# Kernel tuning notes

Hardware: AMD Instinct MI355X
Metric: run time of the kernel (lower is better)

Reference implementation:

```python
import jax, jax.numpy as jnp
from jax import lax
import numpy as np

B, P, D = 32, 196, 2048   # batch, num_pixels (14x14), encoder_dim
A, E, H, V = 512, 512, 512, 10000  # attention_dim, embed_dim, decoder_dim, vocab
L = 21                    # max caption length -> T = 20 decode steps


def setup_inputs() -> dict:
    key = jax.random.key(0)
    ks = jax.random.split(key, 16)
    def n(k, shape, s=0.02):
        return jax.random.normal(k, shape, jnp.float32) * s
    def u(k, shape):
        return jax.random.uniform(k, shape, jnp.float32, -0.1, 0.1)
    caption_lengths = jnp.concatenate(
        [jnp.array([[L]], dtype=jnp.int32),
         jax.random.randint(ks[1], (B - 1, 1), 8, L + 1)], axis=0)
    return dict(
        encoder_out=jax.random.normal(ks[0], (B, P, D), jnp.float32) * 0.5,
        encoded_captions=jax.random.randint(ks[2], (B, L), 0, V),
        caption_lengths=caption_lengths,
        enc_att_w=n(ks[3], (D, A)), enc_att_b=jnp.zeros((A,), jnp.float32),
        dec_att_w=n(ks[4], (H, A)), dec_att_b=jnp.zeros((A,), jnp.float32),
        full_att_w=n(ks[5], (A,)), full_att_b=jnp.zeros((), jnp.float32),
        emb=u(ks[6], (V, E)),
        init_h_w=n(ks[7], (D, H)), init_h_b=jnp.zeros((H,), jnp.float32),
        init_c_w=n(ks[8], (D, H)), init_c_b=jnp.zeros((H,), jnp.float32),
        f_beta_w=n(ks[9], (H, D)), f_beta_b=jnp.zeros((D,), jnp.float32),
        lstm_w_ih=n(ks[10], (E + D, 4 * H)),
        lstm_w_hh=n(ks[11], (H, 4 * H)),
        lstm_b=jnp.zeros((4 * H,), jnp.float32),
        fc_w=u(ks[12], (H, V)), fc_b=jnp.zeros((V,), jnp.float32),
    )


def reference(encoder_out, encoded_captions, caption_lengths,
              enc_att_w, enc_att_b, dec_att_w, dec_att_b, full_att_w, full_att_b,
              emb, init_h_w, init_h_b, init_c_w, init_c_b,
              f_beta_w, f_beta_b, lstm_w_ih, lstm_w_hh, lstm_b, fc_w, fc_b):
    # sort batch by caption length, descending (matches torch .sort descending=True)
    lengths = caption_lengths[:, 0]
    sort_ind = jnp.argsort(-lengths)
    lengths = lengths[sort_ind]
    enc = encoder_out[sort_ind]                 # [B,P,D]
    caps = encoded_captions[sort_ind]           # [B,L]
    embs = emb[caps]                            # [B,L,E]

    mean_enc = enc.mean(axis=1)                 # [B,D]
    h0 = mean_enc @ init_h_w + init_h_b         # [B,H]
    c0 = mean_enc @ init_c_w + init_c_b

    # encoder branch of additive attention is constant across timesteps
    att1 = enc @ enc_att_w + enc_att_b          # [B,P,A]
    dec_lens = lengths - 1                      # [B]
    T = caps.shape[1] - 1

    def step(carry, xs):
        h, c = carry
        emb_t, t = xs                            # [B,E], scalar
        att2 = h @ dec_att_w + dec_att_b         # [B,A]
        e = jnp.einsum('bpa,a->bp', jax.nn.relu(att1 + att2[:, None, :]), full_att_w) + full_att_b
        alpha = jax.nn.softmax(e, axis=1)        # [B,P]
        awe = jnp.einsum('bpd,bp->bd', enc, alpha)
        gate = jax.nn.sigmoid(h @ f_beta_w + f_beta_b)
        awe = gate * awe                         # [B,D]
        x = jnp.concatenate([emb_t, awe], axis=-1)  # [B,E+D]
        g = x @ lstm_w_ih + h @ lstm_w_hh + lstm_b  # [B,4H] gates i,f,g,o
        i_g, f_g, g_g, o_g = jnp.split(g, 4, axis=-1)
        c_new = jax.nn.sigmoid(f_g) * c + jax.nn.sigmoid(i_g) * jnp.tanh(g_g)
        h_new = jax.nn.sigmoid(o_g) * jnp.tanh(c_new)
        preds = h_new @ fc_w + fc_b              # [B,V] (dropout = identity, eval mode)
        active = (t < dec_lens)[:, None]         # length-based batch slicing -> mask
        h = jnp.where(active, h_new, h)
        c = jnp.where(active, c_new, c)
        preds = jnp.where(active, preds, 0.0)
        alpha = jnp.where(active, alpha, 0.0)
        return (h, c), (preds, alpha)

    xs = (jnp.swapaxes(embs[:, :T], 0, 1), jnp.arange(T))
    (_, _), (preds, alphas) = lax.scan(step, (h0, c0), xs)
    predictions = jnp.swapaxes(preds, 0, 1)      # [B,T,V]
    alphas = jnp.swapaxes(alphas, 0, 1)          # [B,T,P]
    return predictions, caps, dec_lens, alphas, sort_ind
```

## Files before the change

kernel.cpp:

```cpp
#include <hip/hip_runtime.h>

#define B_ 32
#define P_ 196
#define D_ 2048
#define A_ 512
#define E_ 512
#define H_ 512
#define V_ 10000
#define L_ 21
#define T_ 20
#define PP 208

typedef unsigned short us;

struct KParams {
  const float* encoder_out; const int* captions; const int* cap_lens;
  const float* enc_att_w; const float* enc_att_b;
  const float* dec_att_w; const float* dec_att_b;
  const float* full_att_w; const float* full_att_b;
  const float* emb;
  const float* init_h_w; const float* init_h_b;
  const float* init_c_w; const float* init_c_b;
  const float* f_beta_w; const float* f_beta_b;
  const float* lstm_w_ih; const float* lstm_w_hh; const float* lstm_b;
  const float* fc_w; const float* fc_b;
  float* out_preds; float* out_caps; float* out_declens; float* out_alphas; float* out_sortind;
  int* sort_ind; int* declen; int* caps_s;
  us* h_bf16; float* c; us* mean_bf16;
  us* waw_bf16; us* wihE_bf16; us* embs_bf16;
  us* att1; us* Wt; us* Wt2; us* Wt3; us* encT; us* awe_bf16;
  float* gpre; float* s1out; float* alpha_g;
  int* sync;
};

__device__ __forceinline__ us f2bf(float x){
  unsigned u = __float_as_uint(x);
  unsigned r = ((u >> 16) & 1u) + 0x7FFFu;
  return (us)((u + r) >> 16);
}
__device__ __forceinline__ unsigned pack2(float a, float b){
  return (unsigned)f2bf(a) | ((unsigned)f2bf(b) << 16);
}
__device__ __forceinline__ float bf2f(unsigned u16){ return __uint_as_float(u16 << 16); }
__device__ __forceinline__ float sigm(float x){ return 1.f/(1.f + __expf(-x)); }
__device__ __forceinline__ float tanh_f(float x){ return 1.f - 2.f/(__expf(2.f*x) + 1.f); }

__device__ __forceinline__ unsigned ald(const unsigned* p){
  return __hip_atomic_load(p, __ATOMIC_RELAXED, __HIP_MEMORY_SCOPE_AGENT);
}
__device__ __forceinline__ void ast(unsigned* p, unsigned v){
  __hip_atomic_store(p, v, __ATOMIC_RELAXED, __HIP_MEMORY_SCOPE_AGENT);
}
__device__ __forceinline__ float aldf(const float* p){
  return __uint_as_float(ald((const unsigned*)p));
}
__device__ __forceinline__ void astf(float* p, float v){
  ast((unsigned*)p, __float_as_uint(v));
}

using bf16x8 = __attribute__((ext_vector_type(8))) short;
using f32x4  = __attribute__((ext_vector_type(4))) float;
#define MFMA(a,b,c) __builtin_amdgcn_mfma_f32_16x16x32_bf16((a),(b),(c),0,0,0)

#define HS 528
#define AS 2064


__global__ void k_meta(KParams p){
  __shared__ int len[32], sidx[32], sdecl[32];
  int tid = threadIdx.x;
  if (tid < 32) len[tid] = p.cap_lens[tid];
  __syncthreads();
  if (tid == 0){
    bool used[32];
    for (int i = 0; i < 32; i++) used[i] = false;
    for (int r = 0; r < 32; r++){
      int best = -1, bl = -2;
      for (int i = 0; i < 32; i++) if (!used[i] && len[i] > bl){ bl = len[i]; best = i; }
      used[best] = true; sidx[r] = best; sdecl[r] = bl - 1;
    }
  }
  __syncthreads();
  if (tid < 32){
    p.sort_ind[tid] = sidx[tid]; p.out_sortind[tid] = (float)sidx[tid];
    p.declen[tid]   = sdecl[tid]; p.out_declens[tid] = (float)sdecl[tid];
  }
  for (int idx = tid; idx < B_*L_; idx += 64){
    int b = idx / L_, l = idx - b*L_;
    int cv = p.captions[sidx[b]*L_ + l];
    p.caps_s[idx] = cv; p.out_caps[idx] = (float)cv;
  }
}

__device__ void tp64(const float* src, us* dst, int R, int C, int Rp, int bi){
  __shared__ float tl[64][68];
  int tilesC = (C + 63) >> 6;
  int tr = bi / tilesC, tc = bi - tr*tilesC;
  int r0 = tr << 6, c0 = tc << 6;
  int tid = threadIdx.x;
  {
    int r = tid >> 2, cs = (tid & 3) << 4;
    bool rok = (r0 + r) < R;
    #pragma unroll
    for (int i = 0; i < 4; i++){
      int c = c0 + cs + i*4;
      float4 v = make_float4(0.f, 0.f, 0.f, 0.f);
      if (rok && c < C) v = *(const float4*)(src + (size_t)(r0 + r)*C + c);
      *(float4*)&tl[r][cs + i*4] = v;
    }
  }
  __syncthreads();
  {
    int c = tid >> 2, rs = (tid & 3) << 4;
    if (c0 + c < C && r0 + rs < Rp){
      us tmp[16];
      #pragma unroll
      for (int i = 0; i < 16; i++) tmp[i] = f2bf(tl[rs + i][c]);
      *(uint4*)(dst + (size_t)(c0 + c)*Rp + r0 + rs)     = *(uint4*)&tmp[0];
      *(uint4*)(dst + (size_t)(c0 + c)*Rp + r0 + rs + 8) = *(uint4*)&tmp[8];
    }
  }
}

__global__ void k_prep(KParams p){
  int bi = blockIdx.x, tid = threadIdx.x;
  if (bi < 512){
    #pragma unroll
    for (int i = 0; i < 4; i++){
      int q = bi*1024 + i*256 + tid;
      const float4* src; uint2* dst; int qq;
      if (q < 262144){ src = (const float4*)p.enc_att_w; dst = (uint2*)p.waw_bf16;  qq = q; }
      else           { src = (const float4*)p.lstm_w_ih; dst = (uint2*)p.wihE_bf16; qq = q - 262144; }
      float4 v = src[qq];
      dst[qq] = make_uint2(pack2(v.x, v.y), pack2(v.z, v.w));
    }
  } else if (bi < 576){   tp64(p.dec_att_w, p.Wt,             512, 512,   512,  bi - 512);
  } else if (bi < 832){   tp64(p.f_beta_w,  p.Wt + 512*512,   512, 2048,  512,  bi - 576);
  } else if (bi < 1088){  tp64(p.lstm_w_hh, p.Wt + 2560*512,  512, 2048,  512,  bi - 832);
  } else if (bi < 2344){  tp64(p.fc_w,      p.Wt + 4608*512,  512, 10000, 512,  bi - 1088);
  } else if (bi < 3368){  tp64(p.lstm_w_ih + 512*2048, p.Wt2, 2048, 2048, 2048, bi - 2344);
  } else if (bi < 3624){  tp64(p.init_h_w,  p.Wt3,            2048, 512,  2048, bi - 3368);
  } else if (bi < 3880){  tp64(p.init_c_w,  p.Wt3 + 512*2048, 2048, 512,  2048, bi - 3624);
  } else if (bi < 4200){
    int q = (bi - 3880)*256 + tid;
    int row = q >> 7, qi = q & 127;
    int t = row >> 5, b = row & 31;
    int cap = p.caps_s[b*L_ + t];
    float4 v = ((const float4*)(p.emb + (size_t)cap*E_))[qi];
    ((uint2*)p.embs_bf16)[q] = make_uint2(pack2(v.x, v.y), pack2(v.z, v.w));
  } else {
    int bl = bi - 4200;
    int b = bl >> 7, ti = bl & 127;
    tp64(p.encoder_out + (size_t)p.sort_ind[b]*(P_*D_), p.encT + (size_t)b*D_*PP,
         196, 2048, PP, ti);
  }
}

__global__ void __launch_bounds__(256) k_gemm2(KParams p){
  __shared__ us a_lds[128][40];
  __shared__ us b_lds[128][40];
  int bi = blockIdx.x;
  const us* Aq = nullptr; const float* Af = nullptr; const int* sidx = nullptr;
  const us* Bq; const float* bias; float* C; int N, K, obf, mode, ti;
  if (bi < 196){
    Af = p.encoder_out; sidx = p.sort_ind; Bq = p.waw_bf16; bias = p.enc_att_b;
    C = (float*)p.att1; N = 512; K = 2048; obf = 1; mode = 1; ti = bi;
  } else {
    Aq = p.embs_bf16; Bq = p.wihE_bf16; bias = p.lstm_b;
    C = p.gpre; N = 2048; K = 512; obf = 0; mode = 0; ti = bi - 196;
  }
  int ntiles = N >> 7;
  int bm = (ti / ntiles) << 7;
  int bn = (ti % ntiles) << 7;
  int tid = threadIdx.x;
  int wave = tid >> 6, lane = tid & 63;
  int wr = (wave >> 1) << 6, wc = (wave & 1) << 6;
  int la = lane & 15, lq = lane >> 4;
  f32x4 acc[4][4] = {};
  for (int k0 = 0; k0 < K; k0 += 32){
    {
      int r = tid >> 1, ch = (tid & 1) << 4;
      if (mode == 0){
        const uint4* asrc = (const uint4*)(Aq + (size_t)(bm + r)*K + k0 + ch);
        uint4 v0 = asrc[0], v1 = asrc[1];
        *(uint4*)&a_lds[r][ch]     = v0;
        *(uint4*)&a_lds[r][ch + 8] = v1;
      } else {
        int g = bm + r; int b = g / 196; int pp = g - b*196;
        const float4* as = (const float4*)(Af + ((size_t)sidx[b]*196 + pp)*2048 + k0 + ch);
        float4 f0 = as[0], f1 = as[1], f2 = as[2], f3 = as[3];
        *(uint4*)&a_lds[r][ch]     = make_uint4(pack2(f0.x,f0.y), pack2(f0.z,f0.w), pack2(f1.x,f1.y), pack2(f1.z,f1.w));
        *(uint4*)&a_lds[r][ch + 8] = make_uint4(pack2(f2.x,f2.y), pack2(f2.z,f2.w), pack2(f3.x,f3.y), pack2(f3.z,f3.w));
      }
      int kk = tid >> 3, n0 = (tid & 7) << 4;
      const us* bs = Bq + (size_t)(k0 + kk)*N + bn + n0;
      uint4 bv0 = *(const uint4*)bs, bv1 = *(const uint4*)(bs + 8);
      unsigned vals[8] = {bv0.x, bv0.y, bv0.z, bv0.w, bv1.x, bv1.y, bv1.z, bv1.w};
      #pragma unroll
      for (int i = 0; i < 8; i++){
        b_lds[n0 + 2*i][kk]     = (us)(vals[i] & 0xffffu);
        b_lds[n0 + 2*i + 1][kk] = (us)(vals[i] >> 16);
      }
    }
    __syncthreads();
    bf16x8 af[4], bfr[4];
    #pragma unroll
    for (int mt = 0; mt < 4; mt++) af[mt]  = *(const bf16x8*)&a_lds[wr + mt*16 + la][lq*8];
    #pragma unroll
    for (int nt = 0; nt < 4; nt++) bfr[nt] = *(const bf16x8*)&b_lds[wc + nt*16 + la][lq*8];
    #pragma unroll
    for (int mt = 0; mt < 4; mt++)
      #pragma unroll
      for (int nt = 0; nt < 4; nt++)
        acc[mt][nt] = MFMA(af[mt], bfr[nt], acc[mt][nt]);
    __syncthreads();
  }
  #pragma unroll
  for (int mt = 0; mt < 4; mt++){
    int row0 = bm + wr + mt*16 + lq*4;
    #pragma unroll
    for (int nt = 0; nt < 4; nt++){
      int coln = bn + wc + nt*16 + la;
      float bb = bias ? bias[coln] : 0.f;
      #pragma unroll
      for (int r = 0; r < 4; r++){
        float v = acc[mt][nt][r] + bb;
        if (obf) ((us*)C)[(size_t)(row0 + r)*N + coln] = f2bf(v);
        else     C[(size_t)(row0 + r)*N + coln] = v;
      }
    }
  }
}


__device__ __forceinline__ void gsync_g(int* sc, int gen, int jb){
  __syncthreads();
  if (threadIdx.x == 0){
    int old = __hip_atomic_fetch_add(&sc[(jb & 7)*32], 1, __ATOMIC_RELEASE, __HIP_MEMORY_SCOPE_AGENT);
    bool last = false;
    if (old == gen*8 - 1){
      int old2 = __hip_atomic_fetch_add(&sc[512], 1, __ATOMIC_RELAXED, __HIP_MEMORY_SCOPE_AGENT);
      if (old2 == gen*8 - 1){
        __hip_atomic_store(&sc[544], gen, __ATOMIC_RELEASE, __HIP_MEMORY_SCOPE_AGENT);
        last = true;
      }
    }
    if (!last){
      while (__hip_atomic_load(&sc[544], __ATOMIC_RELAXED, __HIP_MEMORY_SCOPE_AGENT) < gen)
        __builtin_amdgcn_s_sleep(2);
    }
  }
  __syncthreads();
}

__device__ __forceinline__ void fc_run(const KParams& p, const int* sm_dl, const us* hlds,
                                       int b0, int slot, int nslots, int niter,
                                       int la, int lq, int tpred){
  bf16x8 afr[16];
  #pragma unroll
  for (int ks = 0; ks < 16; ks++) afr[ks] = *(const bf16x8*)&hlds[(la & 7)*HS + lq*8 + ks*32];
  for (int it = 0; it < niter; it++){
    int tile = slot + it*nslots;
    if (tile < 625){
      int n0 = tile*16;
      const us* wp = p.Wt + ((size_t)(4608 + n0 + la))*512 + lq*8;
      f32x4 ac = {};
      #pragma unroll
      for (int ks = 0; ks < 16; ks++){
        bf16x8 bB = *(const bf16x8*)(wp + ks*32);
        ac = MFMA(afr[ks], bB, ac);
      }
      if (lq < 2){
        int v = n0 + la;
        float bb = p.fc_b[v];
        #pragma unroll
        for (int r = 0; r < 4; r++){
          int b = b0 + lq*4 + r;
          bool act = tpred < sm_dl[b];
          p.out_preds[((size_t)b*T_ + tpred)*V_ + v] = act ? (ac[r] + bb) : 0.f;
        }
      }
    }
  }
}

__global__ void __launch_bounds__(512, 2) k_loop(KParams p){
  const int tid = threadIdx.x, blk = blockIdx.x;
  const int gb = blk >> 6, jb = blk & 63, b0 = gb*8;
  const int wv = tid >> 6, lane = tid & 63, la = lane & 15, lq = lane >> 4;
  int* sc = p.sync + gb*1024;
  __shared__ float sm_att2[512], sm_fw[512], sm_red[16];
  __shared__ float sm_a4f[8*PP];
  __shared__ float gq2[4][2][16][8];
  __shared__ int sm_dl[32];
  __shared__ us sm_h[8*HS];
  __shared__ us sm_awe[8*AS];
  int gen = 0;

  if (tid < 32) sm_dl[tid] = p.declen[tid];
  __syncthreads();

  {
    int part = tid & 1, pair = tid >> 1;
    int d = jb*32 + (pair >> 3), b = b0 + (pair & 7);
    const uint4* rp = (const uint4*)(p.encT + ((size_t)b*D_ + d)*PP);
    int cs = part*13;
    float s = 0.f;
    for (int i = cs; i < cs + 13; i++){
      uint4 u = rp[i];
      s += bf2f(u.x&0xffffu)+bf2f(u.x>>16)+bf2f(u.y&0xffffu)+bf2f(u.y>>16)
         + bf2f(u.z&0xffffu)+bf2f(u.z>>16)+bf2f(u.w&0xffffu)+bf2f(u.w>>16);
    }
    s += __shfl_xor(s, 1);
    float mv = s*(1.f/196.f);
    float ov = __shfl_xor(mv, 16);
    if (part == 0 && !(tid & 16))
      ast((unsigned*)p.mean_bf16 + ((size_t)b*1024 + (d >> 1)), pack2(mv, ov));
  }
  gsync_g(sc, ++gen, jb);
  if (jb < 8){
    {
      unsigned* dst = (unsigned*)sm_awe;
      const unsigned* src = (const unsigned*)p.mean_bf16 + (size_t)b0*1024;
      for (int i = tid; i < 8192; i += 512) dst[(i >> 10)*(AS >> 1) + (i & 1023)] = ald(src + i);
    }
    __syncthreads();
    int slot = jb*8 + wv;
    const us* wp = p.Wt3 + ((size_t)(slot*16 + la))*2048 + lq*8;
    const us* ap = sm_awe + (la & 7)*AS + lq*8;
    f32x4 ac0 = {}, ac1 = {};
    for (int ki = 0; ki < 64; ki += 2){
      bf16x8 aA = *(const bf16x8*)(ap + ki*32);
      bf16x8 bB = *(const bf16x8*)(wp + ki*32);
      ac0 = MFMA(aA, bB, ac0);
      bf16x8 aA2 = *(const bf16x8*)(ap + ki*32 + 32);
      bf16x8 bB2 = *(const bf16x8*)(wp + ki*32 + 32);
      ac1 = MFMA(aA2, bB2, ac1);
    }
    f32x4 ac = ac0 + ac1;
    int col = slot*16 + la;
    if (col < 512){
      #pragma unroll
      for (int r = 0; r < 4; r++){
        float v0 = ac[r] + p.init_h_b[col];
        float v1 = __shfl_xor(v0, 1);
        if (lq < 2 && !(la & 1))
          ast((unsigned*)p.h_bf16 + (((size_t)(b0 + lq*4 + r)*512 + col) >> 1), pack2(v0, v1));
      }
    } else {
      #pragma unroll
      for (int r = 0; r < 4; r++)
        if (lq < 2) astf(&p.c[(size_t)(b0 + lq*4 + r)*512 + col - 512], ac[r] + p.init_c_b[col - 512]);
    }
  }
  gsync_g(sc, ++gen, jb);

  for (int t = 0; t < T_; ++t){
    {
      unsigned* dst = (unsigned*)sm_h;
      const unsigned* src = (const unsigned*)p.h_bf16 + (size_t)b0*256;
      for (int i = tid; i < 2048; i += 512) dst[(i >> 8)*(HS >> 1) + (i & 255)] = ald(src + i);
    }
    __syncthreads();
    {
      int slot = jb*8 + wv;
      if (slot < 288){
        bf16x8 afr[16];
        #pragma unroll
        for (int ks = 0; ks < 16; ks++) afr[ks] = *(const bf16x8*)&sm_h[(la & 7)*HS + lq*8 + ks*32];
        int n0 = slot*16;
        const us* wp = p.Wt + ((size_t)(n0 + la))*512 + lq*8;
        f32x4 ac = {};
        #pragma unroll
        for (int ks = 0; ks < 16; ks++){
          bf16x8 bB = *(const bf16x8*)(wp + ks*32);
          ac = MFMA(afr[ks], bB, ac);
        }
        if (lq < 2){
          #pragma unroll
          for (int r = 0; r < 4; r++) astf(&p.s1out[(size_t)(b0 + lq*4 + r)*4608 + n0 + la], ac[r]);
        }
      }
    }
    gsync_g(sc, ++gen, jb);
    if (jb < 8){
      int b = b0 + jb;
      for (int cc = tid; cc < 512; cc += 512){
        sm_att2[cc] = aldf(&p.s1out[(size_t)b*4608 + cc]) + p.dec_att_b[cc];
        sm_fw[cc]   = p.full_att_w[cc];
      }
      __syncthreads();
      float ee = -1e30f;
      if (tid < 196){
        const uint4* row = (const uint4*)(p.att1 + ((size_t)(b*196 + tid))*512);
        float s = 0.f;
        #pragma unroll 8
        for (int i = 0; i < 64; i++){
          uint4 u = row[i];
          float4 a0 = *(const float4*)&sm_att2[i*8], a1 = *(const float4*)&sm_att2[i*8+4];
          float4 f0 = *(const float4*)&sm_fw[i*8],   f1 = *(const float4*)&sm_fw[i*8+4];
          s += fmaxf(bf2f(u.x&0xffffu)+a0.x,0.f)*f0.x + fmaxf(bf2f(u.x>>16)+a0.y,0.f)*f0.y
             + fmaxf(bf2f(u.y&0xffffu)+a0.z,0.f)*f0.z + fmaxf(bf2f(u.y>>16)+a0.w,0.f)*f0.w
             + fmaxf(bf2f(u.z&0xffffu)+a1.x,0.f)*f1.x + fmaxf(bf2f(u.z>>16)+a1.y,0.f)*f1.y
             + fmaxf(bf2f(u.w&0xffffu)+a1.z,0.f)*f1.z + fmaxf(bf2f(u.w>>16)+a1.w,0.f)*f1.w;
        }
        ee = s;
      }
      float v = ee;
      #pragma unroll
      for (int off = 32; off; off >>= 1) v = fmaxf(v, __shfl_xor(v, off));
      if (lane == 0) sm_red[wv] = v;
      __syncthreads();
      float m = sm_red[0];
      #pragma unroll
      for (int i = 1; i < 8; i++) m = fmaxf(m, sm_red[i]);
      float ex = (tid < 196) ? __expf(ee - m) : 0.f;
      float sv = ex;
      #pragma unroll
      for (int off = 32; off; off >>= 1) sv += __shfl_xor(sv, off);
      if (lane == 0) sm_red[8 + wv] = sv;
      __syncthreads();
      float ssum = sm_red[8];
      #pragma unroll
      for (int i = 1; i < 8; i++) ssum += sm_red[8 + i];
      if (tid < 196){
        float a = ex/ssum;
        astf(&p.alpha_g[b*PP + tid], a);
        bool act = t < sm_dl[b];
        p.out_alphas[((size_t)b*T_ + t)*P_ + tid] = act ? a : 0.f;
      } else if (tid < PP) astf(&p.alpha_g[b*PP + tid], 0.f);
    } else if (t > 0){
      fc_run(p, sm_dl, sm_h, b0, (jb - 8)*8 + wv, 448, 2, la, lq, t - 1);
    }
    gsync_g(sc, ++gen, jb);
    {
      for (int i = tid; i < 8*PP; i += 512) sm_a4f[i] = aldf(&p.alpha_g[b0*PP + i]);
      __syncthreads();
      int part = tid & 1, pair = tid >> 1;
      int d = jb*32 + (pair >> 3), b = b0 + (pair & 7);
      const float* al = sm_a4f + (pair & 7)*PP;
      const uint4* rp = (const uint4*)(p.encT + ((size_t)b*D_ + d)*PP);
      int cs = part*13;
      float acc = 0.f;
      for (int i = cs; i < cs + 13; i++){
        uint4 u = rp[i];
        float4 a0 = *(const float4*)(al + i*8), a1 = *(const float4*)(al + i*8 + 4);
        acc += a0.x*bf2f(u.x&0xffffu) + a0.y*bf2f(u.x>>16)
             + a0.z*bf2f(u.y&0xffffu) + a0.w*bf2f(u.y>>16)
             + a1.x*bf2f(u.z&0xffffu) + a1.y*bf2f(u.z>>16)
             + a1.z*bf2f(u.w&0xffffu) + a1.w*bf2f(u.w>>16);
      }
      acc += __shfl_xor(acc, 1);
      float gate = sigm(aldf(&p.s1out[(size_t)b*4608 + 512 + d]) + p.f_beta_b[d]);
      float wv_ = acc*gate;
      float ov = __shfl_xor(wv_, 16);
      if (part == 0 && !(tid & 16))
        ast((unsigned*)p.awe_bf16 + ((size_t)b*1024 + (d >> 1)), pack2(wv_, ov));
    }
    gsync_g(sc, ++gen, jb);
    if (jb < 32){
      {
        unsigned* dst = (unsigned*)sm_awe;
        const unsigned* src = (const unsigned*)p.awe_bf16 + (size_t)b0*1024;
        for (int i = tid; i < 8192; i += 512) dst[(i >> 10)*(AS >> 1) + (i & 1023)] = ald(src + i);
      }
      __syncthreads();
      int q = wv >> 1, kh = wv & 1, hc0 = jb*16;
      const us* wp = p.Wt2 + ((size_t)(q*512 + hc0 + la))*2048 + kh*1024 + lq*8;
      const us* ap = sm_awe + (la & 7)*AS + kh*1024 + lq*8;
      f32x4 ac0 = {}, ac1 = {};
      for (int ki = 0; ki < 32; ki += 2){
        bf16x8 aA = *(const bf16x8*)(ap + ki*32);
        bf16x8 bB = *(const bf16x8*)(wp + ki*32);
        ac0 = MFMA(aA, bB, ac0);
        bf16x8 aA2 = *(const bf16x8*)(ap + ki*32 + 32);
        bf16x8 bB2 = *(const bf16x8*)(wp + ki*32 + 32);
        ac1 = MFMA(aA2, bB2, ac1);
      }
      f32x4 ac = ac0 + ac1;
      if (lq < 2){
        #pragma unroll
        for (int r = 0; r < 4; r++) gq2[q][kh][la][lq*4 + r] = ac[r];
      }
      __syncthreads();
      if (tid < 128){
        int hc = hc0 + (tid & 15), r = tid >> 4;
        int b = b0 + r;
        float gv[4];
        #pragma unroll
        for (int qq = 0; qq < 4; qq++)
          gv[qq] = gq2[qq][0][tid & 15][r] + gq2[qq][1][tid & 15][r]
                 + aldf(&p.s1out[(size_t)b*4608 + 2560 + qq*512 + hc])
                 + p.gpre[((size_t)t*32 + b)*2048 + qq*512 + hc];
        float cold = aldf(&p.c[(size_t)b*512 + hc]);
        float cn = sigm(gv[1])*cold + sigm(gv[0])*tanh_f(gv[2]);
        float hn = sigm(gv[3])*tanh_f(cn);
        float hv1 = __shfl_xor(hn, 1);
        if (t < sm_dl[b]){
          astf(&p.c[(size_t)b*512 + hc], cn);
          if (!(tid & 1))
            ast((unsigned*)p.h_bf16 + (((size_t)b*512 + hc) >> 1), pack2(hn, hv1));
        }
      }
    }
    gsync_g(sc, ++gen, jb);
  }
  {
    unsigned* dst = (unsigned*)sm_h;
    const unsigned* src = (const unsigned*)p.h_bf16 + (size_t)b0*256;
    for (int i = tid; i < 2048; i += 512) dst[(i >> 8)*(HS >> 1) + (i & 255)] = ald(src + i);
  }
  __syncthreads();
  fc_run(p, sm_dl, sm_h, b0, jb*8 + wv, 512, 2, la, lq, T_ - 1);
}


extern "C" void kernel_launch(void* const* d_in, const int* in_sizes, int n_in,
                              void* d_out, int out_size, void* d_ws, size_t ws_size,
                              hipStream_t stream){
  (void)in_sizes; (void)n_in; (void)out_size; (void)ws_size;
  KParams p;
  p.encoder_out = (const float*)d_in[0];
  p.captions    = (const int*)d_in[1];
  p.cap_lens    = (const int*)d_in[2];
  p.enc_att_w   = (const float*)d_in[3];  p.enc_att_b = (const float*)d_in[4];
  p.dec_att_w   = (const float*)d_in[5];  p.dec_att_b = (const float*)d_in[6];
  p.full_att_w  = (const float*)d_in[7];  p.full_att_b = (const float*)d_in[8];
  p.emb         = (const float*)d_in[9];
  p.init_h_w    = (const float*)d_in[10]; p.init_h_b = (const float*)d_in[11];
  p.init_c_w    = (const float*)d_in[12]; p.init_c_b = (const float*)d_in[13];
  p.f_beta_w    = (const float*)d_in[14]; p.f_beta_b = (const float*)d_in[15];
  p.lstm_w_ih   = (const float*)d_in[16]; p.lstm_w_hh = (const float*)d_in[17]; p.lstm_b = (const float*)d_in[18];
  p.fc_w        = (const float*)d_in[19]; p.fc_b = (const float*)d_in[20];

  float* out = (float*)d_out;
  p.out_preds   = out;
  p.out_caps    = out + 6400000;
  p.out_declens = out + 6400672;
  p.out_alphas  = out + 6400704;
  p.out_sortind = out + 6526144;

  char* w = (char*)d_ws; size_t off = 0;
  auto alloc = [&](size_t bytes)->char*{ char* r = w + off; off = (off + bytes + 255) & ~(size_t)255; return r; };
  p.sort_ind  = (int*)alloc(128);
  p.declen    = (int*)alloc(128);
  p.caps_s    = (int*)alloc(2688);
  p.h_bf16    = (us*)alloc(32768);
  p.c         = (float*)alloc(65536);
  p.mean_bf16 = (us*)alloc(131072);
  p.waw_bf16  = (us*)alloc(2097152);
  p.wihE_bf16 = (us*)alloc(2097152);
  p.embs_bf16 = (us*)alloc(655360);
  p.att1      = (us*)alloc(6422528);
  p.Wt        = (us*)alloc(14958592);
  p.Wt2       = (us*)alloc(8388608);
  p.Wt3       = (us*)alloc(4194304);
  p.encT      = (us*)alloc(27262976);
  p.gpre      = (float*)alloc(5242880);
  p.s1out     = (float*)alloc(589824);
  p.alpha_g   = (float*)alloc(26624);
  p.awe_bf16  = (us*)alloc(131072);
  p.sync      = (int*)alloc(32768);

  hipMemsetAsync(p.sync, 0, 32768, stream);
  hipLaunchKernelGGL(k_meta,  dim3(1),    dim3(64),  0, stream, p);
  hipLaunchKernelGGL(k_prep,  dim3(8296), dim3(256), 0, stream, p);
  hipLaunchKernelGGL(k_gemm2, dim3(276),  dim3(256), 0, stream, p);
  void* args[] = { (void*)&p };
  hipLaunchCooperativeKernel((void*)k_loop, dim3(256), dim3(512), args, 0, stream);
}
```

Measured before the change: 1.559 ms.

## Fold weight and encoder transposes into GEMM launch and shrink LDS row padding

The transposes of the recurrent-loop weights and the encoder features are moved out of the prep kernel and into the same launch as the two precompute GEMMs. The GEMM tiles come first in the grid and the transpose blocks follow, so the two kinds of work can overlap and idle tails are cut. Only the bf16 conversions of the embedding and the GEMM-input weights stay in the now smaller first prep kernel. The LDS row strides HS/AS are also reduced, which changes bank-conflict behavior and LDS footprint in the loop kernel.

```diff
diff --git a/kernel.cpp b/kernel.cpp
--- a/kernel.cpp
+++ b/kernel.cpp
@@ -62,8 +62,8 @@
 using f32x4  = __attribute__((ext_vector_type(4))) float;
 #define MFMA(a,b,c) __builtin_amdgcn_mfma_f32_16x16x32_bf16((a),(b),(c),0,0,0)
 
-#define HS 528
-#define AS 2064
+#define HS 520
+#define AS 2056
 
 
 __global__ void k_meta(KParams p){
@@ -122,7 +122,7 @@
   }
 }
 
-__global__ void k_prep(KParams p){
+__global__ void k_prep1(KParams p){
   int bi = blockIdx.x, tid = threadIdx.x;
   if (bi < 512){
     #pragma unroll
@@ -134,32 +134,37 @@
       float4 v = src[qq];
       dst[qq] = make_uint2(pack2(v.x, v.y), pack2(v.z, v.w));
     }
-  } else if (bi < 576){   tp64(p.dec_att_w, p.Wt,             512, 512,   512,  bi - 512);
-  } else if (bi < 832){   tp64(p.f_beta_w,  p.Wt + 512*512,   512, 2048,  512,  bi - 576);
-  } else if (bi < 1088){  tp64(p.lstm_w_hh, p.Wt + 2560*512,  512, 2048,  512,  bi - 832);
-  } else if (bi < 2344){  tp64(p.fc_w,      p.Wt + 4608*512,  512, 10000, 512,  bi - 1088);
-  } else if (bi < 3368){  tp64(p.lstm_w_ih + 512*2048, p.Wt2, 2048, 2048, 2048, bi - 2344);
-  } else if (bi < 3624){  tp64(p.init_h_w,  p.Wt3,            2048, 512,  2048, bi - 3368);
-  } else if (bi < 3880){  tp64(p.init_c_w,  p.Wt3 + 512*2048, 2048, 512,  2048, bi - 3624);
-  } else if (bi < 4200){
-    int q = (bi - 3880)*256 + tid;
+  } else {
+    int q = (bi - 512)*256 + tid;
     int row = q >> 7, qi = q & 127;
     int t = row >> 5, b = row & 31;
     int cap = p.caps_s[b*L_ + t];
     float4 v = ((const float4*)(p.emb + (size_t)cap*E_))[qi];
     ((uint2*)p.embs_bf16)[q] = make_uint2(pack2(v.x, v.y), pack2(v.z, v.w));
-  } else {
-    int bl = bi - 4200;
-    int b = bl >> 7, ti = bl & 127;
-    tp64(p.encoder_out + (size_t)p.sort_ind[b]*(P_*D_), p.encT + (size_t)b*D_*PP,
-         196, 2048, PP, ti);
-  }
-}
-
-__global__ void __launch_bounds__(256) k_gemm2(KParams p){
+  }
+}
+
+__global__ void __launch_bounds__(256) k_big(KParams p){
+  int bi = blockIdx.x, tid = threadIdx.x;
+  if (bi >= 276){
+    int bj = bi - 276;
+    if      (bj < 64)   tp64(p.dec_att_w, p.Wt,             512, 512,   512,  bj);
+    else if (bj < 320)  tp64(p.f_beta_w,  p.Wt + 512*512,   512, 2048,  512,  bj - 64);
+    else if (bj < 576)  tp64(p.lstm_w_hh, p.Wt + 2560*512,  512, 2048,  512,  bj - 320);
+    else if (bj < 1832) tp64(p.fc_w,      p.Wt + 4608*512,  512, 10000, 512,  bj - 576);
+    else if (bj < 2856) tp64(p.lstm_w_ih + 512*2048, p.Wt2, 2048, 2048, 2048, bj - 1832);
+    else if (bj < 3112) tp64(p.init_h_w,  p.Wt3,            2048, 512,  2048, bj - 2856);
+    else if (bj < 3368) tp64(p.init_c_w,  p.Wt3 + 512*2048, 2048, 512,  2048, bj - 3112);
+    else {
+      int bl = bj - 3368;
+      int b = bl >> 7, ti = bl & 127;
+      tp64(p.encoder_out + (size_t)p.sort_ind[b]*(P_*D_), p.encT + (size_t)b*D_*PP,
+           196, 2048, PP, ti);
+    }
+    return;
+  }
   __shared__ us a_lds[128][40];
   __shared__ us b_lds[128][40];
-  int bi = blockIdx.x;
   const us* Aq = nullptr; const float* Af = nullptr; const int* sidx = nullptr;
   const us* Bq; const float* bias; float* C; int N, K, obf, mode, ti;
   if (bi < 196){
@@ -172,7 +177,6 @@
   int ntiles = N >> 7;
   int bm = (ti / ntiles) << 7;
   int bn = (ti % ntiles) << 7;
-  int tid = threadIdx.x;
   int wave = tid >> 6, lane = tid & 63;
   int wr = (wave >> 1) << 6, wc = (wave & 1) << 6;
   int la = lane & 15, lq = lane >> 4;
@@ -564,8 +568,8 @@
 
   hipMemsetAsync(p.sync, 0, 32768, stream);
   hipLaunchKernelGGL(k_meta,  dim3(1),    dim3(64),  0, stream, p);
-  hipLaunchKernelGGL(k_prep,  dim3(8296), dim3(256), 0, stream, p);
-  hipLaunchKernelGGL(k_gemm2, dim3(276),  dim3(256), 0, stream, p);
+  hipLaunchKernelGGL(k_prep1, dim3(832),  dim3(256), 0, stream, p);
+  hipLaunchKernelGGL(k_big,   dim3(7740), dim3(256), 0, stream, p);
   void* args[] = { (void*)&p };
   hipLaunchCooperativeKernel((void*)k_loop, dim3(256), dim3(512), args, 0, stream);
 }
```

New measurement: 1.523 ms. 1.02x faster.
